# Kernel optimization log

Hardware: AMD Instinct MI355X
Metric: run time of the kernel (lower is better)

The kernel has to match this reference:

```python
import jax, jax.numpy as jnp
import numpy as np

HEAD_NUM = 8


def setup_inputs() -> dict:
    key = jax.random.key(0)
    ks = jax.random.split(key, 12)
    B, H, W, D = 8, 32, 32, 256
    Dh = D  # depth is even -> D_h = depth
    inner = Dh * HEAD_NUM
    s = 0.02
    inp = {
        "x": jax.random.normal(ks[0], (B, H, W, D), jnp.float32),
        "Kw": jax.random.normal(ks[1], (D, inner), jnp.float32) * s,
        "Kb": jnp.zeros((inner,), jnp.float32),
        "Qw": jax.random.normal(ks[2], (D, inner), jnp.float32) * s,
        "Qb": jnp.zeros((inner,), jnp.float32),
        "Vw": jax.random.normal(ks[3], (D, inner), jnp.float32) * s,
        "Vb": jnp.zeros((inner,), jnp.float32),
        "Pw": jax.random.normal(ks[4], (inner, D), jnp.float32) * s,
        "Pb": jnp.zeros((D,), jnp.float32),
        "row_tab": jax.random.normal(ks[5], (2 * H - 1, Dh // 2), jnp.float32) * s,
        "col_tab": jax.random.normal(ks[6], (2 * W - 1, Dh // 2), jnp.float32) * s,
    }
    return inp


def reference(x, Kw, Kb, Qw, Qb, Vw, Vb, Pw, Pb, row_tab, col_tab):
    B, H, W, D = x.shape
    hn = HEAD_NUM
    Dh = Kw.shape[1] // hn
    half = Dh // 2

    K = (x @ Kw + Kb).reshape(B, H, W, hn, Dh)
    Q = (x @ Qw + Qb).reshape(B, H, W, hn, Dh)
    V = (x @ Vw + Vb).reshape(B, H, W, hn, Dh)

    # content-content logits: [B,H,W,hn,H,W]
    score = jnp.einsum('bijhd,bklhd->bijhkl', Q, K)

    # relative row/col position bias via learned embeddings
    row_mat = jnp.arange(H)[None, :] - jnp.arange(H)[:, None] + H - 1  # (H,H)
    col_mat = jnp.arange(W)[:, None] - jnp.arange(W)[None, :] + W - 1  # (W,W)
    row_emb = row_tab[row_mat]  # (H,H,half)
    col_emb = col_tab[col_mat]  # (W,W,half)
    row_score = jnp.einsum('bijhd,ikd->bijhk', Q[..., :half], row_emb)[..., :, None]
    col_score = jnp.einsum('bijhd,jkd->bijhk', Q[..., half:], col_emb)[..., None, :]
    score = score + row_score + col_score

    attn = jax.nn.softmax(score.reshape(B, H, W, hn, H * W), axis=-1)
    attn = attn.reshape(B, H, W, hn, H, W)

    attended = jnp.einsum('bijhkl,bklhd->bijhd', attn, V).reshape(B, H, W, hn * Dh)
    return attended @ Pw + Pb
```

## Files before the change

kernel.cpp:

```cpp
#include <hip/hip_runtime.h>

typedef __attribute__((ext_vector_type(8))) short short8;
typedef __attribute__((ext_vector_type(4))) float f32x4;
typedef __attribute__((ext_vector_type(2))) unsigned int u32x2;
typedef __attribute__((ext_vector_type(4))) unsigned int u32x4;

__device__ __forceinline__ unsigned short f2bf(float f) {
  unsigned u = __float_as_uint(f);
  u += 0x7FFF + ((u >> 16) & 1);
  return (unsigned short)(u >> 16);
}
__device__ __forceinline__ unsigned packbf(float a, float b) {
  return (unsigned)f2bf(a) | ((unsigned)f2bf(b) << 16);
}
__device__ __forceinline__ float bf2f(unsigned short s) {
  return __uint_as_float(((unsigned)s) << 16);
}
__device__ __forceinline__ f32x4 mfma16(short8 a, short8 b, f32x4 c) {
  return __builtin_amdgcn_mfma_f32_16x16x32_bf16(a, b, c, 0, 0, 0);
}

typedef __attribute__((address_space(3))) unsigned int lds_u32;
typedef __attribute__((address_space(1))) const unsigned int glb_u32;
__device__ __forceinline__ void gll16(const void* g, void* l) {
  __builtin_amdgcn_global_load_lds((glb_u32*)g, (lds_u32*)l, 16, 0, 0);
}

__global__ void cvt_x_kernel(const float* __restrict__ in, unsigned short* __restrict__ out, int n) {
  int i = blockIdx.x * 256 + threadIdx.x;
  if (i < n) out[i] = f2bf(in[i]);
}

__global__ void transpose_cvt_kernel(const float* __restrict__ in, unsigned short* __restrict__ out,
                                     int K, int N) {
  int i = blockIdx.x * 256 + threadIdx.x;
  if (i < K * N) {
    int n = i / K, k = i - n * K;
    out[i] = f2bf(in[(size_t)k * N + n]);
  }
}

template<int MODE, int BMI>
__global__ __launch_bounds__(256, 2) void gemm128(const unsigned short* __restrict__ A,
    const unsigned short* __restrict__ BT, const float* __restrict__ bias,
    void* __restrict__ Cout, int Mdim, int Ndim, int Kdim) {
  constexpr int BM = 64 * BMI, MI = 2 * BMI;
  __shared__ __align__(16) short As[BM * 32];
  __shared__ __align__(16) short Bs[128 * 32];
  const int tid = threadIdx.x;
  const int wid = tid >> 6, lane = tid & 63;
  const int l15 = lane & 15, lg = lane >> 4;
  const int m0 = blockIdx.y * BM, n0 = blockIdx.x * 128;
  const int wr = (wid >> 1) * (BM / 2), wc = (wid & 1) * 64;
  const int srow = lane >> 2, schunk = (lane & 3) * 8;
  const f32x4 z = {0.f, 0.f, 0.f, 0.f};
  f32x4 acc[MI][4];
#pragma unroll
  for (int mi = 0; mi < MI; ++mi)
#pragma unroll
    for (int ni = 0; ni < 4; ++ni) acc[mi][ni] = z;

  for (int kt = 0; kt < Kdim; kt += 32) {
#pragma unroll
    for (int i = 0; i < BMI; ++i) {
      int r0 = wid * (BM / 4) + i * 16;
      gll16(A + (size_t)(m0 + r0 + srow) * Kdim + kt + schunk, &As[r0 * 32]);
    }
#pragma unroll
    for (int i = 0; i < 2; ++i) {
      int r0 = wid * 32 + i * 16;
      gll16(BT + (size_t)(n0 + r0 + srow) * Kdim + kt + schunk, &Bs[r0 * 32]);
    }
    __syncthreads();
    short8 a[MI], b[4];
#pragma unroll
    for (int mi = 0; mi < MI; ++mi) a[mi] = *(const short8*)&As[(wr + mi * 16 + l15) * 32 + lg * 8];
#pragma unroll
    for (int ni = 0; ni < 4; ++ni) b[ni] = *(const short8*)&Bs[(wc + ni * 16 + l15) * 32 + lg * 8];
#pragma unroll
    for (int mi = 0; mi < MI; ++mi)
#pragma unroll
      for (int ni = 0; ni < 4; ++ni)
        acc[mi][ni] = mfma16(a[mi], b[ni], acc[mi][ni]);
    __syncthreads();
  }
#pragma unroll
  for (int mi = 0; mi < MI; ++mi)
#pragma unroll
    for (int ni = 0; ni < 4; ++ni)
#pragma unroll
      for (int e = 0; e < 4; ++e) {
        int gm = m0 + wr + mi * 16 + lg * 4 + e;
        int gn = n0 + wc + ni * 16 + l15;
        float v = acc[mi][ni][e] + bias[gn];
        if (MODE == 0) {
          ((unsigned short*)Cout)[(size_t)gm * Ndim + gn] = f2bf(v);
        } else if (MODE == 1) {
          ((float*)Cout)[(size_t)gm * Ndim + gn] = v;
        } else {
          int b_ = gm >> 10, pos = gm & 1023;
          int h = gn >> 8, d = gn & 255;
          ((unsigned short*)Cout)[((size_t)((b_ * 8 + h) * 256 + d)) * 1024 + pos] = f2bf(v);
        }
      }
}

__global__ __launch_bounds__(256, 4) void bias_mfma_kernel(const unsigned short* __restrict__ Q,
    const float* __restrict__ row_tab, const float* __restrict__ col_tab,
    float* __restrict__ Rb, float* __restrict__ Cb) {
  const int side = blockIdx.y >> 5;
  const int ij = blockIdx.y & 31;
  const int q4 = blockIdx.x;
  const int tid = threadIdx.x, wv = tid >> 6, lane = tid & 63;
  const int l15 = lane & 15, lg = lane >> 4;
  const float* tab = side ? col_tab : row_tab;
  const int doff = side ? 128 : 0;
  float* outp = side ? Cb : Rb;

  short8 eb[2][4];
#pragma unroll
  for (int nf = 0; nf < 2; ++nf) {
    int k = nf * 16 + l15;
    int trow = side ? (ij - k + 31) : (k - ij + 31);
    const float* tp = tab + (size_t)trow * 128 + lg * 8;
#pragma unroll
    for (int ks = 0; ks < 4; ++ks) {
      float4 f0 = *(const float4*)(tp + ks * 32);
      float4 f1 = *(const float4*)(tp + ks * 32 + 4);
      u32x4 r;
      r.x = packbf(f0.x, f0.y);
      r.y = packbf(f0.z, f0.w);
      r.z = packbf(f1.x, f1.y);
      r.w = packbf(f1.z, f1.w);
      eb[nf][ks] = *(short8*)&r;
    }
  }

  const f32x4 z = {0.f, 0.f, 0.f, 0.f};
  const int rbase = q4 * 512 + wv * 128;
#pragma unroll
  for (int mf = 0; mf < 8; ++mf) {
    int r = rbase + mf * 16 + l15;
    int b = r >> 8, jj = (r >> 3) & 31, h = r & 7;
    int q = side ? (jj * 32 + ij) : (ij * 32 + jj);
    const unsigned short* ap = Q + (size_t)(b * 1024 + q) * 2048 + h * 256 + doff + lg * 8;
    short8 af[4];
#pragma unroll
    for (int ks = 0; ks < 4; ++ks) af[ks] = *(const short8*)(ap + ks * 32);
    f32x4 a0 = z, a1 = z;
#pragma unroll
    for (int ks = 0; ks < 4; ++ks) {
      a0 = mfma16(af[ks], eb[0][ks], a0);
      a1 = mfma16(af[ks], eb[1][ks], a1);
    }
#pragma unroll
    for (int e = 0; e < 4; ++e) {
      int r2 = rbase + mf * 16 + lg * 4 + e;
      int b2 = r2 >> 8, jj2 = (r2 >> 3) & 31, h2 = r2 & 7;
      int q2 = side ? (jj2 * 32 + ij) : (ij * 32 + jj2);
      float* op = outp + ((size_t)((b2 * 8 + h2) * 1024 + q2)) * 32 + l15;
      op[0] = a0[e];
      op[16] = a1[e];
    }
  }
}

__global__ __launch_bounds__(512, 2) void attn_kernel(const unsigned short* __restrict__ Q,
    const unsigned short* __restrict__ K, const unsigned short* __restrict__ Vt,
    const float* __restrict__ Rb, const float* __restrict__ Cb,
    unsigned short* __restrict__ Att) {
  __shared__ __align__(16) char KV[4][32768];
  __shared__ unsigned short RbL[256 * 32];
  const int wgid = blockIdx.x;
  const int bh = (wgid & 7) * 8 + ((wgid >> 3) & 7);
  const int qblk = wgid >> 6;
  const int b = bh >> 3, h = bh & 7;
  const int tid = threadIdx.x, wv = tid >> 6, lane = tid & 63;
  const int l15 = lane & 15, lg = lane >> 4;
  const int q0w = qblk * 256 + wv * 32;

  const unsigned short* kbase = K + (size_t)(b * 1024) * 2048 + h * 256;
  const unsigned short* vbase = Vt + (size_t)bh * 256 * 1024;

  auto stage = [&](int buf, int t) {
#pragma unroll
    for (int it = 0; it < 2; ++it) {
      int s = it * 8192 + wv * 1024 + lane * 16;
      int key = s >> 9;
      int c = ((s >> 4) & 31) ^ (key & 7);
      gll16(kbase + (size_t)(t * 32 + key) * 2048 + c * 8, &KV[buf][it * 8192 + wv * 1024]);
    }
#pragma unroll
    for (int it = 0; it < 2; ++it) {
      int s = it * 8192 + wv * 1024 + lane * 16;
      int r = s >> 9;
      int cc = ((s >> 4) & 31) ^ (r & 7);
      int d = r * 8 + (cc >> 2);
      gll16(vbase + (size_t)d * 1024 + t * 32 + (cc & 3) * 8,
            &KV[buf][16384 + it * 8192 + wv * 1024]);
    }
  };

  stage(0, 0);
  stage(1, 1);

  short8 qa[2][8];
#pragma unroll
  for (int qf = 0; qf < 2; ++qf) {
    const unsigned short* qp = Q + (size_t)(b * 1024 + q0w + qf * 16 + l15) * 2048 + h * 256;
#pragma unroll
    for (int kk = 0; kk < 8; ++kk) qa[qf][kk] = *(const short8*)(qp + kk * 32 + lg * 8);
  }
  float4 cpre[2][2];
#pragma unroll
  for (int qf = 0; qf < 2; ++qf) {
    const float* cbp = Cb + ((size_t)bh * 1024 + q0w + qf * 16 + l15) * 32;
    cpre[qf][0] = *(const float4*)(cbp + lg * 4);
    cpre[qf][1] = *(const float4*)(cbp + 16 + lg * 4);
  }
  {
    const float* rsrc = Rb + ((size_t)bh * 1024 + qblk * 256) * 32;
#pragma unroll
    for (int i = 0; i < 16; ++i) {
      int idx = i * 512 + tid;
      RbL[idx] = f2bf(rsrc[idx]);
    }
  }
  asm volatile("s_waitcnt lgkmcnt(0)" ::: "memory");

  const f32x4 z = {0.f, 0.f, 0.f, 0.f};
  f32x4 o[16][2];
#pragma unroll
  for (int nf2 = 0; nf2 < 16; ++nf2) { o[nf2][0] = z; o[nf2][1] = z; }
  float m_r[2] = {-1e30f, -1e30f}, l_r[2] = {0.f, 0.f};

  const int nfd = lg >> 1;
  const int srcA = ((lg & 1) * 2) * 16 + l15, srcB = srcA + 16;
  const unsigned short* rbl0 = &RbL[(wv * 32 + l15) * 32];
  const unsigned short* rbl1 = rbl0 + 16 * 32;

  for (int t = 0; t < 32; ++t) {
    if (t < 30) stage((t + 2) & 3, t + 2);
    if (t < 30)       asm volatile("s_waitcnt vmcnt(8)" ::: "memory");
    else if (t == 30) asm volatile("s_waitcnt vmcnt(4)" ::: "memory");
    else              asm volatile("s_waitcnt vmcnt(0)" ::: "memory");
    __builtin_amdgcn_s_barrier();
    asm volatile("" ::: "memory");

    const char* kb = &KV[t & 3][0];
    const char* vb = &KV[t & 3][16384];

    f32x4 s[2][2] = {{z, z}, {z, z}};
#pragma unroll
    for (int kk = 0; kk < 8; ++kk) {
      int c0 = (kk * 4 + lg) ^ (l15 & 7);
      short8 k0 = *(const short8*)(kb + l15 * 512 + c0 * 16);
      int key1 = 16 + l15;
      int c1 = (kk * 4 + lg) ^ (key1 & 7);
      short8 k1 = *(const short8*)(kb + key1 * 512 + c1 * 16);
      s[0][0] = mfma16(k0, qa[0][kk], s[0][0]);
      s[1][0] = mfma16(k0, qa[1][kk], s[1][0]);
      s[0][1] = mfma16(k1, qa[0][kk], s[0][1]);
      s[1][1] = mfma16(k1, qa[1][kk], s[1][1]);
    }
    float rb0 = bf2f(rbl0[t]), rb1 = bf2f(rbl1[t]);
#pragma unroll
    for (int nf = 0; nf < 2; ++nf)
#pragma unroll
      for (int e = 0; e < 4; ++e) {
        s[0][nf][e] += rb0 + ((const float*)&cpre[0][nf])[e];
        s[1][nf][e] += rb1 + ((const float*)&cpre[1][nf])[e];
      }
    float tm[2];
#pragma unroll
    for (int qf = 0; qf < 2; ++qf) {
      float m2 = fmaxf(fmaxf(s[qf][0][0], s[qf][0][1]), fmaxf(s[qf][0][2], s[qf][0][3]));
#pragma unroll
      for (int e = 0; e < 4; ++e) m2 = fmaxf(m2, s[qf][1][e]);
      m2 = fmaxf(m2, __shfl_xor(m2, 16));
      m2 = fmaxf(m2, __shfl_xor(m2, 32));
      tm[qf] = m2;
    }
    if (__any((tm[0] > m_r[0] + 8.f) || (tm[1] > m_r[1] + 8.f))) {
#pragma unroll
      for (int qf = 0; qf < 2; ++qf) {
        float mn = fmaxf(m_r[qf], tm[qf]);
        float sc = __expf(m_r[qf] - mn);
        m_r[qf] = mn;
        l_r[qf] *= sc;
#pragma unroll
        for (int nf2 = 0; nf2 < 16; ++nf2)
#pragma unroll
          for (int e = 0; e < 4; ++e) o[nf2][qf][e] *= sc;
      }
    }
    short8 pb[2];
#pragma unroll
    for (int qf = 0; qf < 2; ++qf) {
      float ps = 0.f;
#pragma unroll
      for (int nf = 0; nf < 2; ++nf)
#pragma unroll
        for (int e = 0; e < 4; ++e) {
          float pv = __expf(s[qf][nf][e] - m_r[qf]);
          s[qf][nf][e] = pv;
          ps += pv;
        }
      ps += __shfl_xor(ps, 16);
      ps += __shfl_xor(ps, 32);
      l_r[qf] += ps;
      unsigned u0 = packbf(s[qf][0][0], s[qf][0][1]);
      unsigned u1 = packbf(s[qf][0][2], s[qf][0][3]);
      unsigned u2 = packbf(s[qf][1][0], s[qf][1][1]);
      unsigned u3 = packbf(s[qf][1][2], s[qf][1][3]);
      unsigned a0 = __shfl(u0, srcA), b0 = __shfl(u2, srcA);
      unsigned a1 = __shfl(u1, srcA), b1 = __shfl(u3, srcA);
      unsigned a2 = __shfl(u0, srcB), b2 = __shfl(u2, srcB);
      unsigned a3 = __shfl(u1, srcB), b3 = __shfl(u3, srcB);
      u32x4 r4;
      r4.x = nfd ? b0 : a0;
      r4.y = nfd ? b1 : a1;
      r4.z = nfd ? b2 : a2;
      r4.w = nfd ? b3 : a3;
      pb[qf] = *(short8*)&r4;
    }
#pragma unroll
    for (int nf2 = 0; nf2 < 16; ++nf2) {
      int d = nf2 * 16 + l15;
      int r = d >> 3;
      int cc = ((d & 7) * 4 + lg) ^ (r & 7);
      short8 vf = *(const short8*)(vb + r * 512 + cc * 16);
      o[nf2][0] = mfma16(vf, pb[0], o[nf2][0]);
      o[nf2][1] = mfma16(vf, pb[1], o[nf2][1]);
    }
  }
#pragma unroll
  for (int qf = 0; qf < 2; ++qf) {
    unsigned short* op = Att + (size_t)(b * 1024 + q0w + qf * 16 + l15) * 2048 + h * 256;
    float inv = 1.f / l_r[qf];
#pragma unroll
    for (int nf2 = 0; nf2 < 16; ++nf2) {
      u32x2 w;
      w.x = packbf(o[nf2][qf][0] * inv, o[nf2][qf][1] * inv);
      w.y = packbf(o[nf2][qf][2] * inv, o[nf2][qf][3] * inv);
      *(u32x2*)(op + nf2 * 16 + lg * 4) = w;
    }
  }
}

extern "C" void kernel_launch(void* const* d_in, const int* in_sizes, int n_in,
                              void* d_out, int out_size, void* d_ws, size_t ws_size,
                              hipStream_t stream) {
  (void)in_sizes; (void)n_in; (void)out_size;
  const float* x   = (const float*)d_in[0];
  const float* Kw  = (const float*)d_in[1];
  const float* Kb  = (const float*)d_in[2];
  const float* Qw  = (const float*)d_in[3];
  const float* Qb  = (const float*)d_in[4];
  const float* Vw  = (const float*)d_in[5];
  const float* Vb  = (const float*)d_in[6];
  const float* Pw  = (const float*)d_in[7];
  const float* Pb  = (const float*)d_in[8];
  const float* row_tab = (const float*)d_in[9];
  const float* col_tab = (const float*)d_in[10];
  float* out = (float*)d_out;

  char* ws = (char*)d_ws;
  size_t off = 0;
  auto alloc = [&](size_t bytes) { char* p = ws + off; off += bytes; return p; };
  unsigned short* Xb   = (unsigned short*)alloc((size_t)8192 * 256 * 2);
  unsigned short* WqT  = (unsigned short*)alloc((size_t)2048 * 256 * 2);
  unsigned short* WkT  = (unsigned short*)alloc((size_t)2048 * 256 * 2);
  unsigned short* WvT  = (unsigned short*)alloc((size_t)2048 * 256 * 2);
  unsigned short* PwT  = (unsigned short*)alloc((size_t)256 * 2048 * 2);
  unsigned short* Qg   = (unsigned short*)alloc((size_t)8192 * 2048 * 2);
  unsigned short* Kg   = (unsigned short*)alloc((size_t)8192 * 2048 * 2);
  unsigned short* VtG  = (unsigned short*)alloc((size_t)8192 * 2048 * 2);
  unsigned short* AttG = (unsigned short*)alloc((size_t)8192 * 2048 * 2);
  float* Rb = (float*)alloc((size_t)64 * 1024 * 32 * 4);
  float* Cb = (float*)alloc((size_t)64 * 1024 * 32 * 4);
  if (off > ws_size) return;

  cvt_x_kernel<<<8192, 256, 0, stream>>>(x, Xb, 8192 * 256);
  transpose_cvt_kernel<<<2048, 256, 0, stream>>>(Qw, WqT, 256, 2048);
  transpose_cvt_kernel<<<2048, 256, 0, stream>>>(Kw, WkT, 256, 2048);
  transpose_cvt_kernel<<<2048, 256, 0, stream>>>(Vw, WvT, 256, 2048);
  transpose_cvt_kernel<<<2048, 256, 0, stream>>>(Pw, PwT, 2048, 256);

  gemm128<0, 2><<<dim3(16, 64), 256, 0, stream>>>(Xb, WqT, Qb, Qg, 8192, 2048, 256);
  gemm128<0, 2><<<dim3(16, 64), 256, 0, stream>>>(Xb, WkT, Kb, Kg, 8192, 2048, 256);
  gemm128<2, 2><<<dim3(16, 64), 256, 0, stream>>>(Xb, WvT, Vb, VtG, 8192, 2048, 256);

  bias_mfma_kernel<<<dim3(4, 64), 256, 0, stream>>>(Qg, row_tab, col_tab, Rb, Cb);
  attn_kernel<<<256, 512, 0, stream>>>(Qg, Kg, VtG, Rb, Cb, AttG);
  gemm128<1, 1><<<dim3(2, 128), 256, 0, stream>>>(AttG, PwT, Pb, out, 8192, 256, 2048);
}
```

Baseline: 288.2 us.

## Use 64-key tiles with double buffering and MFMA-based row-sum in attention

The attention loop now processes 64 keys per iteration instead of 32, staging K and V into two 64 KB buffers rather than four 32 KB buffers, with a barrier at the end of each iteration. The softmax denominator is accumulated through an MFMA against a ones vector, replacing the shuffle-based reductions. The row-bias table is transposed in LDS for per-tile lookup, and s_setprio is raised around the MFMA sections. This halves the number of loop iterations and barriers, but reduces the prefetch depth to one tile ahead and adds an extra barrier per step.

After: 407.3 us. 1.41x slower.

```diff
diff --git a/kernel.cpp b/kernel.cpp
--- a/kernel.cpp
+++ b/kernel.cpp
@@ -169,8 +169,8 @@
     const unsigned short* __restrict__ K, const unsigned short* __restrict__ Vt,
     const float* __restrict__ Rb, const float* __restrict__ Cb,
     unsigned short* __restrict__ Att) {
-  __shared__ __align__(16) char KV[4][32768];
-  __shared__ unsigned short RbL[256 * 32];
+  __shared__ __align__(16) char KV[2][65536];
+  __shared__ unsigned short RbL[32 * 256];
   const int wgid = blockIdx.x;
   const int bh = (wgid & 7) * 8 + ((wgid >> 3) & 7);
   const int qblk = wgid >> 6;
@@ -184,25 +184,25 @@
 
   auto stage = [&](int buf, int t) {
 #pragma unroll
-    for (int it = 0; it < 2; ++it) {
+    for (int it = 0; it < 4; ++it) {
       int s = it * 8192 + wv * 1024 + lane * 16;
       int key = s >> 9;
       int c = ((s >> 4) & 31) ^ (key & 7);
-      gll16(kbase + (size_t)(t * 32 + key) * 2048 + c * 8, &KV[buf][it * 8192 + wv * 1024]);
-    }
-#pragma unroll
-    for (int it = 0; it < 2; ++it) {
+      gll16(kbase + (size_t)(t * 64 + key) * 2048 + c * 8, &KV[buf][it * 8192 + wv * 1024]);
+    }
+#pragma unroll
+    for (int it = 0; it < 4; ++it) {
       int s = it * 8192 + wv * 1024 + lane * 16;
       int r = s >> 9;
-      int cc = ((s >> 4) & 31) ^ (r & 7);
-      int d = r * 8 + (cc >> 2);
-      gll16(vbase + (size_t)d * 1024 + t * 32 + (cc & 3) * 8,
-            &KV[buf][16384 + it * 8192 + wv * 1024]);
+      int slot = ((s >> 4) & 31) ^ (r & 7);
+      int d = r * 4 + (slot & 3);
+      int kc = slot >> 2;
+      gll16(vbase + (size_t)d * 1024 + t * 64 + kc * 8,
+            &KV[buf][32768 + it * 8192 + wv * 1024]);
     }
   };
 
   stage(0, 0);
-  stage(1, 1);
 
   short8 qa[2][8];
 #pragma unroll
@@ -223,7 +223,8 @@
 #pragma unroll
     for (int i = 0; i < 16; ++i) {
       int idx = i * 512 + tid;
-      RbL[idx] = f2bf(rsrc[idx]);
+      int q = idx >> 5, kr = idx & 31;
+      RbL[kr * 256 + q] = f2bf(rsrc[idx]);
     }
   }
   asm volatile("s_waitcnt lgkmcnt(0)" ::: "memory");
@@ -232,51 +233,63 @@
   f32x4 o[16][2];
 #pragma unroll
   for (int nf2 = 0; nf2 < 16; ++nf2) { o[nf2][0] = z; o[nf2][1] = z; }
-  float m_r[2] = {-1e30f, -1e30f}, l_r[2] = {0.f, 0.f};
+  f32x4 o_l[2] = {z, z};
+  float m_r[2] = {-1e30f, -1e30f};
 
   const int nfd = lg >> 1;
   const int srcA = ((lg & 1) * 2) * 16 + l15, srcB = srcA + 16;
-  const unsigned short* rbl0 = &RbL[(wv * 32 + l15) * 32];
-  const unsigned short* rbl1 = rbl0 + 16 * 32;
-
-  for (int t = 0; t < 32; ++t) {
-    if (t < 30) stage((t + 2) & 3, t + 2);
-    if (t < 30)       asm volatile("s_waitcnt vmcnt(8)" ::: "memory");
-    else if (t == 30) asm volatile("s_waitcnt vmcnt(4)" ::: "memory");
-    else              asm volatile("s_waitcnt vmcnt(0)" ::: "memory");
+  u32x4 onesu;
+  onesu.x = onesu.y = onesu.z = onesu.w = 0x3F803F80u;
+  const short8 ones = *(short8*)&onesu;
+
+  for (int t = 0; t < 16; ++t) {
+    if (t < 15) stage((t + 1) & 1, t + 1);
+    if (t < 15) asm volatile("s_waitcnt vmcnt(8)" ::: "memory");
+    else        asm volatile("s_waitcnt vmcnt(0)" ::: "memory");
     __builtin_amdgcn_s_barrier();
     asm volatile("" ::: "memory");
 
-    const char* kb = &KV[t & 3][0];
-    const char* vb = &KV[t & 3][16384];
-
-    f32x4 s[2][2] = {{z, z}, {z, z}};
+    const char* kb = &KV[t & 1][0];
+    const char* vb = &KV[t & 1][32768];
+
+    f32x4 s[2][4];
+#pragma unroll
+    for (int qf = 0; qf < 2; ++qf)
+#pragma unroll
+      for (int nf = 0; nf < 4; ++nf) s[qf][nf] = z;
+    __builtin_amdgcn_s_setprio(1);
 #pragma unroll
     for (int kk = 0; kk < 8; ++kk) {
-      int c0 = (kk * 4 + lg) ^ (l15 & 7);
-      short8 k0 = *(const short8*)(kb + l15 * 512 + c0 * 16);
-      int key1 = 16 + l15;
-      int c1 = (kk * 4 + lg) ^ (key1 & 7);
-      short8 k1 = *(const short8*)(kb + key1 * 512 + c1 * 16);
-      s[0][0] = mfma16(k0, qa[0][kk], s[0][0]);
-      s[1][0] = mfma16(k0, qa[1][kk], s[1][0]);
-      s[0][1] = mfma16(k1, qa[0][kk], s[0][1]);
-      s[1][1] = mfma16(k1, qa[1][kk], s[1][1]);
-    }
-    float rb0 = bf2f(rbl0[t]), rb1 = bf2f(rbl1[t]);
-#pragma unroll
-    for (int nf = 0; nf < 2; ++nf)
-#pragma unroll
-      for (int e = 0; e < 4; ++e) {
-        s[0][nf][e] += rb0 + ((const float*)&cpre[0][nf])[e];
-        s[1][nf][e] += rb1 + ((const float*)&cpre[1][nf])[e];
-      }
+#pragma unroll
+      for (int nf = 0; nf < 4; ++nf) {
+        int key = nf * 16 + l15;
+        int c0 = (kk * 4 + lg) ^ (key & 7);
+        short8 kf = *(const short8*)(kb + key * 512 + c0 * 16);
+        s[0][nf] = mfma16(kf, qa[0][kk], s[0][nf]);
+        s[1][nf] = mfma16(kf, qa[1][kk], s[1][nf]);
+      }
+    }
+    __builtin_amdgcn_s_setprio(0);
+    float rbv[2][2];
+    rbv[0][0] = bf2f(RbL[(2 * t) * 256 + wv * 32 + l15]);
+    rbv[0][1] = bf2f(RbL[(2 * t + 1) * 256 + wv * 32 + l15]);
+    rbv[1][0] = bf2f(RbL[(2 * t) * 256 + wv * 32 + 16 + l15]);
+    rbv[1][1] = bf2f(RbL[(2 * t + 1) * 256 + wv * 32 + 16 + l15]);
+#pragma unroll
+    for (int qf = 0; qf < 2; ++qf)
+#pragma unroll
+      for (int nf = 0; nf < 4; ++nf)
+#pragma unroll
+        for (int e = 0; e < 4; ++e)
+          s[qf][nf][e] += rbv[qf][nf >> 1] + ((const float*)&cpre[qf][nf & 1])[e];
     float tm[2];
 #pragma unroll
     for (int qf = 0; qf < 2; ++qf) {
-      float m2 = fmaxf(fmaxf(s[qf][0][0], s[qf][0][1]), fmaxf(s[qf][0][2], s[qf][0][3]));
-#pragma unroll
-      for (int e = 0; e < 4; ++e) m2 = fmaxf(m2, s[qf][1][e]);
+      float m2 = s[qf][0][0];
+#pragma unroll
+      for (int nf = 0; nf < 4; ++nf)
+#pragma unroll
+        for (int e = 0; e < 4; ++e) m2 = fmaxf(m2, s[qf][nf][e]);
       m2 = fmaxf(m2, __shfl_xor(m2, 16));
       m2 = fmaxf(m2, __shfl_xor(m2, 32));
       tm[qf] = m2;
@@ -287,57 +300,69 @@
         float mn = fmaxf(m_r[qf], tm[qf]);
         float sc = __expf(m_r[qf] - mn);
         m_r[qf] = mn;
-        l_r[qf] *= sc;
+#pragma unroll
+        for (int e = 0; e < 4; ++e) o_l[qf][e] *= sc;
 #pragma unroll
         for (int nf2 = 0; nf2 < 16; ++nf2)
 #pragma unroll
           for (int e = 0; e < 4; ++e) o[nf2][qf][e] *= sc;
       }
     }
-    short8 pb[2];
+    short8 pb[2][2];
 #pragma unroll
     for (int qf = 0; qf < 2; ++qf) {
-      float ps = 0.f;
-#pragma unroll
-      for (int nf = 0; nf < 2; ++nf)
-#pragma unroll
-        for (int e = 0; e < 4; ++e) {
-          float pv = __expf(s[qf][nf][e] - m_r[qf]);
-          s[qf][nf][e] = pv;
-          ps += pv;
-        }
-      ps += __shfl_xor(ps, 16);
-      ps += __shfl_xor(ps, 32);
-      l_r[qf] += ps;
-      unsigned u0 = packbf(s[qf][0][0], s[qf][0][1]);
-      unsigned u1 = packbf(s[qf][0][2], s[qf][0][3]);
-      unsigned u2 = packbf(s[qf][1][0], s[qf][1][1]);
-      unsigned u3 = packbf(s[qf][1][2], s[qf][1][3]);
-      unsigned a0 = __shfl(u0, srcA), b0 = __shfl(u2, srcA);
-      unsigned a1 = __shfl(u1, srcA), b1 = __shfl(u3, srcA);
-      unsigned a2 = __shfl(u0, srcB), b2 = __shfl(u2, srcB);
-      unsigned a3 = __shfl(u1, srcB), b3 = __shfl(u3, srcB);
-      u32x4 r4;
-      r4.x = nfd ? b0 : a0;
-      r4.y = nfd ? b1 : a1;
-      r4.z = nfd ? b2 : a2;
-      r4.w = nfd ? b3 : a3;
-      pb[qf] = *(short8*)&r4;
-    }
+#pragma unroll
+      for (int nf = 0; nf < 4; ++nf)
+#pragma unroll
+        for (int e = 0; e < 4; ++e)
+          s[qf][nf][e] = __expf(s[qf][nf][e] - m_r[qf]);
+      unsigned u[4][2];
+#pragma unroll
+      for (int nf = 0; nf < 4; ++nf) {
+        u[nf][0] = packbf(s[qf][nf][0], s[qf][nf][1]);
+        u[nf][1] = packbf(s[qf][nf][2], s[qf][nf][3]);
+      }
+#pragma unroll
+      for (int kk = 0; kk < 2; ++kk) {
+        unsigned a0 = __shfl(u[2 * kk][0], srcA), b0 = __shfl(u[2 * kk + 1][0], srcA);
+        unsigned a1 = __shfl(u[2 * kk][1], srcA), b1 = __shfl(u[2 * kk + 1][1], srcA);
+        unsigned a2 = __shfl(u[2 * kk][0], srcB), b2 = __shfl(u[2 * kk + 1][0], srcB);
+        unsigned a3 = __shfl(u[2 * kk][1], srcB), b3 = __shfl(u[2 * kk + 1][1], srcB);
+        u32x4 r4;
+        r4.x = nfd ? b0 : a0;
+        r4.y = nfd ? b1 : a1;
+        r4.z = nfd ? b2 : a2;
+        r4.w = nfd ? b3 : a3;
+        pb[qf][kk] = *(short8*)&r4;
+      }
+    }
+    __builtin_amdgcn_s_setprio(1);
+    o_l[0] = mfma16(ones, pb[0][0], o_l[0]);
+    o_l[0] = mfma16(ones, pb[0][1], o_l[0]);
+    o_l[1] = mfma16(ones, pb[1][0], o_l[1]);
+    o_l[1] = mfma16(ones, pb[1][1], o_l[1]);
 #pragma unroll
     for (int nf2 = 0; nf2 < 16; ++nf2) {
       int d = nf2 * 16 + l15;
-      int r = d >> 3;
-      int cc = ((d & 7) * 4 + lg) ^ (r & 7);
-      short8 vf = *(const short8*)(vb + r * 512 + cc * 16);
-      o[nf2][0] = mfma16(vf, pb[0], o[nf2][0]);
-      o[nf2][1] = mfma16(vf, pb[1], o[nf2][1]);
-    }
+      int r = d >> 2;
+      int d3 = d & 3;
+#pragma unroll
+      for (int s2 = 0; s2 < 2; ++s2) {
+        int slot = ((s2 * 4 + lg) << 2) | d3;
+        int cc = slot ^ (r & 7);
+        short8 vf = *(const short8*)(vb + r * 512 + cc * 16);
+        o[nf2][0] = mfma16(vf, pb[0][s2], o[nf2][0]);
+        o[nf2][1] = mfma16(vf, pb[1][s2], o[nf2][1]);
+      }
+    }
+    __builtin_amdgcn_s_setprio(0);
+    asm volatile("" ::: "memory");
+    __builtin_amdgcn_s_barrier();
   }
 #pragma unroll
   for (int qf = 0; qf < 2; ++qf) {
     unsigned short* op = Att + (size_t)(b * 1024 + q0w + qf * 16 + l15) * 2048 + h * 256;
-    float inv = 1.f / l_r[qf];
+    float inv = 1.f / o_l[qf][0];
 #pragma unroll
     for (int nf2 = 0; nf2 < 16; ++nf2) {
       u32x2 w;
```
